# Kernel tuning notes

Measured on AMD Instinct MI355X. Metric: run time of the kernel, lower is better.

## Reference

```python
import jax, jax.numpy as jnp
import numpy as np

# 5-tap binomial kernel, same as torch module
_H5 = jnp.array([0.0625, 0.25, 0.375, 0.25, 0.0625], dtype=jnp.float32)
_K1 = _H5[:, None] * _H5[None, :]        # 5x5 Gaussian, sums to 1 (reduce kernel)
_K4 = 4.0 * _K1                           # expand kernel (gain 4)
# polyphase sub-kernels for expand (match torch strided slicing of kernel)
_KER00 = _K4[0::2, 0::2]  # 3x3
_KER01 = _K4[0::2, 1::2]  # 3x2
_KER10 = _K4[1::2, 0::2]  # 2x3
_KER11 = _K4[1::2, 1::2]  # 2x2


def _dwconv(x, k, stride=1):
    """Depthwise valid conv, same kernel per channel. x: NCHW, k: (kh, kw)."""
    C = x.shape[1]
    kern = jnp.broadcast_to(k[None, None].astype(x.dtype), (C, 1) + k.shape)
    return jax.lax.conv_general_dilated(
        x, kern, (stride, stride), 'VALID',
        dimension_numbers=('NCHW', 'OIHW', 'NCHW'),
        feature_group_count=C)


def pyr_reduce(im):
    # replicate-pad 2 each side, 5x5 conv, subsample [0::2,0::2] == stride-2 conv
    x = jnp.pad(im, ((0, 0), (0, 0), (2, 2), (2, 2)), mode='edge')
    return _dwconv(x, _K1, stride=2)


def pyr_expand(im):
    B, C, H, W = im.shape
    x_r2c2 = jnp.pad(im, ((0, 0), (0, 0), (1, 1), (1, 1)), mode='edge')  # top+bot, left+right
    x_r2c1 = jnp.pad(im, ((0, 0), (0, 0), (1, 1), (0, 1)), mode='edge')  # top+bot, right
    x_c2r1 = jnp.pad(im, ((0, 0), (0, 0), (0, 1), (1, 1)), mode='edge')  # bot, left+right
    x_c1r1 = jnp.pad(im, ((0, 0), (0, 0), (0, 1), (0, 1)), mode='edge')  # bot, right
    o00 = _dwconv(x_r2c2, _KER00)  # -> out[0::2, 0::2]
    o01 = _dwconv(x_r2c1, _KER01)  # -> out[0::2, 1::2]
    o10 = _dwconv(x_c2r1, _KER10)  # -> out[1::2, 0::2]
    o11 = _dwconv(x_c1r1, _KER11)  # -> out[1::2, 1::2]
    out = jnp.zeros((B, C, 2 * H, 2 * W), im.dtype)
    out = out.at[:, :, 0::2, 0::2].set(o00)
    out = out.at[:, :, 0::2, 1::2].set(o01)
    out = out.at[:, :, 1::2, 0::2].set(o10)
    out = out.at[:, :, 1::2, 1::2].set(o11)
    return out


def setup_inputs() -> dict:
    key = jax.random.key(0)
    im = jax.random.normal(key, (16, 3, 1024, 1024), dtype=jnp.float32)
    return {"im": im, "levels": 5}


def reference(im, levels):
    gpyr = [im]
    for _ in range(levels - 1):
        gpyr.append(pyr_reduce(gpyr[-1]))
    lpyr = [gpyr[l] - pyr_expand(gpyr[l + 1]) for l in range(levels - 1)]
    lpyr.append(gpyr[-1])
    return tuple(lpyr)
```

## Files before the change

kernel.cpp:

```cpp
#include <hip/hip_runtime.h>


#define RBX 64
#define RBY 4

typedef float fx4 __attribute__((ext_vector_type(4)));

template <bool EDGE>
__device__ __forceinline__ void reduce_accum(const float* __restrict__ src,
                                             int Hin, int Win, int rbase, int cb,
                                             float (&acc)[4][4]) {
    const float w0 = 0.0625f, w1 = 0.25f, w2 = 0.375f;
    const float wr[5] = {w0, w1, w2, w1, w0};
#pragma unroll
    for (int rr = 0; rr < 11; ++rr) {
        int gr = rbase + rr;
        gr = gr < 0 ? 0 : (gr > Hin - 1 ? Hin - 1 : gr);
        const float* row = src + (size_t)gr * Win;
        float v[16];
        if (!EDGE) {
#pragma unroll
            for (int q = 0; q < 4; ++q) {
                fx4 f = *reinterpret_cast<const fx4*>(row + cb + 4 * q);
                v[4 * q + 0] = f.x; v[4 * q + 1] = f.y;
                v[4 * q + 2] = f.z; v[4 * q + 3] = f.w;
            }
        } else {
#pragma unroll
            for (int c = 0; c < 16; ++c) {
                int gc = cb + c;
                gc = gc < 0 ? 0 : (gc > Win - 1 ? Win - 1 : gc);
                v[c] = row[gc];
            }
        }
        float h[4];
#pragma unroll
        for (int c = 0; c < 4; ++c) {
            const float* vv = v + 2 + 2 * c;
            float s04 = vv[0] + vv[4];
            float s13 = vv[1] + vv[3];
            float hh = w0 * s04;
            hh = fmaf(w1, s13, hh);
            hh = fmaf(w2, vv[2], hh);
            h[c] = hh;
        }
#pragma unroll
        for (int i = 0; i < 4; ++i) {
            const int a = rr - 2 * i;
            if (a >= 0 && a <= 4) {
                const float w = wr[a];
#pragma unroll
                for (int c = 0; c < 4; ++c)
                    acc[i][c] = fmaf(w, h[c], acc[i][c]);
            }
        }
    }
}

__device__ __forceinline__ void reduce_block(const float* __restrict__ src,
                                             float* __restrict__ dst,
                                             int Hin, int Win, int Hout, int Wout,
                                             int bx, int by, int tx, int ty) {
    const int t = bx * RBX + tx;
    const int i0 = (by * RBY + ty) * 4;
    const int j0 = 4 * t;
    if (j0 >= Wout || i0 >= Hout) return;

    const int cb = 8 * t - 4;
    const int rbase = 2 * i0 - 2;
    const bool edge = (cb < 0) | (cb + 15 > Win - 1);

    float acc[4][4];
#pragma unroll
    for (int i = 0; i < 4; ++i)
#pragma unroll
        for (int c = 0; c < 4; ++c) acc[i][c] = 0.f;

    if (!edge) reduce_accum<false>(src, Hin, Win, rbase, cb, acc);
    else       reduce_accum<true>(src, Hin, Win, rbase, cb, acc);

    float* drow = dst + j0;
#pragma unroll
    for (int i = 0; i < 4; ++i) {
        fx4 o = {acc[i][0], acc[i][1], acc[i][2], acc[i][3]};
        *reinterpret_cast<fx4*>(drow + (size_t)(i0 + i) * Wout) = o;
    }
}

__launch_bounds__(256)
__global__ void reduce_kernel(const float* __restrict__ in, float* __restrict__ out,
                              int Hin, int Win, int Hout, int Wout) {
    const int p = blockIdx.z;
    reduce_block(in + (size_t)p * Hin * Win, out + (size_t)p * Hout * Wout,
                 Hin, Win, Hout, Wout, blockIdx.x, blockIdx.y, threadIdx.x, threadIdx.y);
}

template <bool NT>
__device__ __forceinline__ fx4 ld4(const float* p) {
    if (NT) return __builtin_nontemporal_load(reinterpret_cast<const fx4*>(p));
    return *reinterpret_cast<const fx4*>(p);
}
template <bool NT>
__device__ __forceinline__ void st4(float* p, fx4 v) {
    if (NT) __builtin_nontemporal_store(v, reinterpret_cast<fx4*>(p));
    else    *reinterpret_cast<fx4*>(p) = v;
}

template <bool NT>
__device__ __forceinline__ void lap_block(const float* __restrict__ fine,
                                          const float* __restrict__ coarse,
                                          float* __restrict__ out,
                                          int Hc, int Wc, int bx, int by, int tx, int ty) {
    const int t = bx * 64 + tx;
    const int i = by * 4 + ty;
    if (i >= Hc || t >= (Wc >> 2)) return;

    const int im1 = i > 0 ? i - 1 : 0;
    const int ip1 = i < Hc - 1 ? i + 1 : Hc - 1;
    const float* rm = coarse + (size_t)im1 * Wc;
    const float* r0 = coarse + (size_t)i   * Wc;
    const float* rp = coarse + (size_t)ip1 * Wc;

    const int jl = 4 * t - 1 > 0 ? 4 * t - 1 : 0;
    const int jr = 4 * t + 4 < Wc - 1 ? 4 * t + 4 : Wc - 1;

    float cm[6], c0[6], cp[6];
    {
        fx4 m = *reinterpret_cast<const fx4*>(rm + 4 * t);
        fx4 z = *reinterpret_cast<const fx4*>(r0 + 4 * t);
        fx4 q = *reinterpret_cast<const fx4*>(rp + 4 * t);
        cm[1] = m.x; cm[2] = m.y; cm[3] = m.z; cm[4] = m.w;
        c0[1] = z.x; c0[2] = z.y; c0[3] = z.z; c0[4] = z.w;
        cp[1] = q.x; cp[2] = q.y; cp[3] = q.z; cp[4] = q.w;
        cm[0] = rm[jl]; cm[5] = rm[jr];
        c0[0] = r0[jl]; c0[5] = r0[jr];
        cp[0] = rp[jl]; cp[5] = rp[jr];
    }

    float e[6], o[6];
#pragma unroll
    for (int c = 0; c < 6; ++c) {
        e[c] = fmaf(0.125f, cm[c], fmaf(0.75f, c0[c], 0.125f * cp[c]));
        o[c] = 0.5f * (c0[c] + cp[c]);
    }

    float ev[8], ov[8];
#pragma unroll
    for (int q = 0; q < 4; ++q) {
        ev[2 * q]     = fmaf(0.125f, e[q], fmaf(0.75f, e[q + 1], 0.125f * e[q + 2]));
        ev[2 * q + 1] = 0.5f * (e[q + 1] + e[q + 2]);
        ov[2 * q]     = fmaf(0.125f, o[q], fmaf(0.75f, o[q + 1], 0.125f * o[q + 2]));
        ov[2 * q + 1] = 0.5f * (o[q + 1] + o[q + 2]);
    }

    const int Wf = 2 * Wc;
    const size_t r0off = (size_t)(2 * i) * Wf + 8 * t;
    const float* f0 = fine + r0off;
    const float* f1 = f0 + Wf;
    fx4 a0 = ld4<NT>(f0), a1 = ld4<NT>(f0 + 4);
    fx4 b0 = ld4<NT>(f1), b1 = ld4<NT>(f1 + 4);

    float* w0 = out + r0off;
    float* w1 = w0 + Wf;
    fx4 o0 = {a0.x - ev[0], a0.y - ev[1], a0.z - ev[2], a0.w - ev[3]};
    fx4 o1 = {a1.x - ev[4], a1.y - ev[5], a1.z - ev[6], a1.w - ev[7]};
    fx4 o2 = {b0.x - ov[0], b0.y - ov[1], b0.z - ov[2], b0.w - ov[3]};
    fx4 o3 = {b1.x - ov[4], b1.y - ov[5], b1.z - ov[6], b1.w - ov[7]};
    st4<NT>(w0,     o0);
    st4<NT>(w0 + 4, o1);
    st4<NT>(w1,     o2);
    st4<NT>(w1 + 4, o3);
}

__launch_bounds__(256)
__global__ void lap_kernel(const float* __restrict__ fine, const float* __restrict__ coarse,
                           float* __restrict__ out, int Hc, int Wc) {
    const int p = blockIdx.z;
    const size_t mplane = (size_t)Hc * Wc;
    lap_block<false>(fine + (size_t)p * 4 * mplane, coarse + (size_t)p * mplane,
                     out + (size_t)p * 4 * mplane, Hc, Wc,
                     blockIdx.x, blockIdx.y, threadIdx.x, threadIdx.y);
}

template <bool NT>
__launch_bounds__(256)
__global__ void fused_kernel(const float* __restrict__ fine, const float* __restrict__ mid,
                             float* __restrict__ lap_dst, float* __restrict__ red_dst,
                             int Hc, int Wc, int ylap) {
    const int p = blockIdx.z;
    const size_t mplane = (size_t)Hc * Wc;
    if ((int)blockIdx.y < ylap) {
        lap_block<NT>(fine + (size_t)p * 4 * mplane, mid + (size_t)p * mplane,
                      lap_dst + (size_t)p * 4 * mplane, Hc, Wc,
                      blockIdx.x, blockIdx.y, threadIdx.x, threadIdx.y);
    } else {
        reduce_block(mid + (size_t)p * mplane, red_dst + (size_t)p * (mplane >> 2),
                     Hc, Wc, Hc >> 1, Wc >> 1,
                     blockIdx.x, (int)blockIdx.y - ylap, threadIdx.x, threadIdx.y);
    }
}

extern "C" void kernel_launch(void* const* d_in, const int* in_sizes, int n_in,
                              void* d_out, int out_size, void* d_ws, size_t ws_size,
                              hipStream_t stream) {
    (void)in_sizes; (void)n_in; (void)d_ws; (void)ws_size; (void)out_size;
    const float* im = (const float*)d_in[0];
    float* out = (float*)d_out;

    const int P = 48;
    const int H0 = 1024, W0 = 1024;

    size_t off[5];
    size_t acc = 0;
    for (int l = 0; l < 5; ++l) {
        off[l] = acc;
        int h = H0 >> l, w = W0 >> l;
        acc += (size_t)P * h * w;
    }

    {
        int Hout = H0 >> 1, Wout = W0 >> 1;
        dim3 blk(RBX, RBY, 1);
        dim3 grid((Wout + 255) / 256, (Hout + 15) / 16, P);
        reduce_kernel<<<grid, blk, 0, stream>>>(im, out + off[1], H0, W0, Hout, Wout);
    }

    for (int l = 0; l < 3; ++l) {
        int Hc = H0 >> (l + 1), Wc = W0 >> (l + 1);
        int xlap = (Wc / 4 + 63) / 64, ylap = (Hc + 3) / 4;
        int Hout = Hc >> 1, Wout = Wc >> 1;
        int xred = (Wout + 255) / 256, yred = (Hout + 15) / 16;
        dim3 blk(64, 4, 1);
        dim3 grid(xlap > xred ? xlap : xred, ylap + yred, P);
        const float* fine = (l == 0) ? im : (out + off[l]);
        if (l == 0)
            fused_kernel<true><<<grid, blk, 0, stream>>>(fine, out + off[l + 1],
                                                         out + off[l], out + off[l + 2],
                                                         Hc, Wc, ylap);
        else
            fused_kernel<false><<<grid, blk, 0, stream>>>(fine, out + off[l + 1],
                                                          out + off[l], out + off[l + 2],
                                                          Hc, Wc, ylap);
    }

    {
        int Hc = H0 >> 4, Wc = W0 >> 4;
        dim3 blk(64, 4, 1);
        dim3 grid((Wc / 4 + 63) / 64, (Hc + 3) / 4, P);
        lap_kernel<<<grid, blk, 0, stream>>>(out + off[3], out + off[4], out + off[3], Hc, Wc);
    }
}
```

Baseline: 487.6 us.

## Replace multi-kernel pyramid launches with one persistent kernel using grid barriers

Adds a persistent pyr_kernel with 1024 blocks that walk each pyramid stage in grid-stride loops and separate the stages with an atomic-counter global barrier held in the workspace. This removes the four separate kernel launches and their inter-kernel gaps and tail effects. The cost is barrier spin overhead and reliance on all 1024 blocks being co-resident (launch bounds of 4 blocks per CU). The barrier has a spin timeout, so if residency is not met, correctness could break silently. It also adds a memset per call.

```diff
diff --git a/kernel.cpp b/kernel.cpp
--- a/kernel.cpp
+++ b/kernel.cpp
@@ -1,8 +1,5 @@
 #include <hip/hip_runtime.h>
 
-
-#define RBX 64
-#define RBY 4
 
 typedef float fx4 __attribute__((ext_vector_type(4)));
 
@@ -61,8 +58,8 @@
                                              float* __restrict__ dst,
                                              int Hin, int Win, int Hout, int Wout,
                                              int bx, int by, int tx, int ty) {
-    const int t = bx * RBX + tx;
-    const int i0 = (by * RBY + ty) * 4;
+    const int t = bx * 64 + tx;
+    const int i0 = (by * 4 + ty) * 4;
     const int j0 = 4 * t;
     if (j0 >= Wout || i0 >= Hout) return;
 
@@ -85,14 +82,6 @@
         fx4 o = {acc[i][0], acc[i][1], acc[i][2], acc[i][3]};
         *reinterpret_cast<fx4*>(drow + (size_t)(i0 + i) * Wout) = o;
     }
-}
-
-__launch_bounds__(256)
-__global__ void reduce_kernel(const float* __restrict__ in, float* __restrict__ out,
-                              int Hin, int Win, int Hout, int Wout) {
-    const int p = blockIdx.z;
-    reduce_block(in + (size_t)p * Hin * Win, out + (size_t)p * Hout * Wout,
-                 Hin, Win, Hout, Wout, blockIdx.x, blockIdx.y, threadIdx.x, threadIdx.y);
 }
 
 template <bool NT>
@@ -170,6 +159,105 @@
     st4<NT>(w0 + 4, o1);
     st4<NT>(w1,     o2);
     st4<NT>(w1 + 4, o3);
+}
+
+__device__ __forceinline__ void gbar(unsigned* ctr, unsigned target) {
+    __syncthreads();
+    if (threadIdx.x == 0 && threadIdx.y == 0) {
+        __threadfence();
+        __hip_atomic_fetch_add(ctr, 1u, __ATOMIC_ACQ_REL, __HIP_MEMORY_SCOPE_AGENT);
+        unsigned spins = 0;
+        while (__hip_atomic_load(ctr, __ATOMIC_ACQUIRE, __HIP_MEMORY_SCOPE_AGENT) < target) {
+            __builtin_amdgcn_s_sleep(8);
+            if (++spins > 2000000u) break;
+        }
+        __threadfence();
+    }
+    __syncthreads();
+}
+
+#define OFF1 50331648UL
+#define OFF2 62914560UL
+#define OFF3 66060288UL
+#define OFF4 66846720UL
+
+__launch_bounds__(256, 4)
+__global__ void pyr_kernel(const float* __restrict__ im, float* __restrict__ out,
+                           unsigned* ctr) {
+    const int tx = threadIdx.x, ty = threadIdx.y;
+    const unsigned gsz = gridDim.x;
+    const unsigned nblk = gsz;
+
+    for (unsigned bt = blockIdx.x; bt < 3072; bt += gsz) {
+        unsigned p = bt >> 6, r = bt & 63;
+        reduce_block(im + (size_t)p * (1024 * 1024), out + OFF1 + (size_t)p * (512 * 512),
+                     1024, 1024, 512, 512, r & 1, r >> 1, tx, ty);
+    }
+    gbar(ctr, nblk * 1);
+
+    for (unsigned bt = blockIdx.x; bt < 13056; bt += gsz) {
+        if (bt < 12288) {
+            unsigned p = bt >> 8, r = bt & 255;
+            lap_block<true>(im + (size_t)p * (1024 * 1024),
+                            out + OFF1 + (size_t)p * (512 * 512),
+                            out + (size_t)p * (1024 * 1024),
+                            512, 512, r & 1, r >> 1, tx, ty);
+        } else {
+            unsigned b2 = bt - 12288;
+            unsigned p = b2 >> 4, r = b2 & 15;
+            reduce_block(out + OFF1 + (size_t)p * (512 * 512), out + OFF2 + (size_t)p * (256 * 256),
+                         512, 512, 256, 256, 0, r, tx, ty);
+        }
+    }
+    gbar(ctr, nblk * 2);
+
+    for (unsigned bt = blockIdx.x; bt < 3456; bt += gsz) {
+        if (bt < 3072) {
+            unsigned p = bt >> 6, by = bt & 63;
+            lap_block<false>(out + OFF1 + (size_t)p * (512 * 512),
+                             out + OFF2 + (size_t)p * (256 * 256),
+                             out + OFF1 + (size_t)p * (512 * 512),
+                             256, 256, 0, by, tx, ty);
+        } else {
+            unsigned b2 = bt - 3072;
+            unsigned p = b2 >> 3, r = b2 & 7;
+            reduce_block(out + OFF2 + (size_t)p * (256 * 256), out + OFF3 + (size_t)p * (128 * 128),
+                         256, 256, 128, 128, 0, r, tx, ty);
+        }
+    }
+    gbar(ctr, nblk * 3);
+
+    for (unsigned bt = blockIdx.x; bt < 1728; bt += gsz) {
+        if (bt < 1536) {
+            unsigned p = bt >> 5, by = bt & 31;
+            lap_block<false>(out + OFF2 + (size_t)p * (256 * 256),
+                             out + OFF3 + (size_t)p * (128 * 128),
+                             out + OFF2 + (size_t)p * (256 * 256),
+                             128, 128, 0, by, tx, ty);
+        } else {
+            unsigned b2 = bt - 1536;
+            unsigned p = b2 >> 2, r = b2 & 3;
+            reduce_block(out + OFF3 + (size_t)p * (128 * 128), out + OFF4 + (size_t)p * (64 * 64),
+                         128, 128, 64, 64, 0, r, tx, ty);
+        }
+    }
+    gbar(ctr, nblk * 4);
+
+    for (unsigned bt = blockIdx.x; bt < 768; bt += gsz) {
+        unsigned p = bt >> 4, by = bt & 15;
+        lap_block<false>(out + OFF3 + (size_t)p * (128 * 128),
+                         out + OFF4 + (size_t)p * (64 * 64),
+                         out + OFF3 + (size_t)p * (128 * 128),
+                         64, 64, 0, by, tx, ty);
+    }
+}
+
+__launch_bounds__(256)
+__global__ void reduce_kernel(const float* __restrict__ in, float* __restrict__ out,
+                              int Hin, int Win, int Hout, int Wout) {
+    const int p = blockIdx.z;
+    reduce_block(in + (size_t)p * Hin * Win, out + (size_t)p * Hout * Wout,
+                 Hin, Win, Hout, Wout, blockIdx.x, blockIdx.y, threadIdx.x, threadIdx.y);
 }
 
 __launch_bounds__(256)
@@ -203,13 +291,19 @@
 extern "C" void kernel_launch(void* const* d_in, const int* in_sizes, int n_in,
                               void* d_out, int out_size, void* d_ws, size_t ws_size,
                               hipStream_t stream) {
-    (void)in_sizes; (void)n_in; (void)d_ws; (void)ws_size; (void)out_size;
+    (void)in_sizes; (void)n_in; (void)out_size;
     const float* im = (const float*)d_in[0];
     float* out = (float*)d_out;
 
+    if (d_ws != nullptr && ws_size >= 64) {
+        hipMemsetAsync(d_ws, 0, 64, stream);
+        unsigned* ctr = (unsigned*)d_ws;
+        pyr_kernel<<<dim3(1024, 1, 1), dim3(64, 4, 1), 0, stream>>>(im, out, ctr);
+        return;
+    }
+
     const int P = 48;
     const int H0 = 1024, W0 = 1024;
-
     size_t off[5];
     size_t acc = 0;
     for (int l = 0; l < 5; ++l) {
@@ -217,14 +311,12 @@
         int h = H0 >> l, w = W0 >> l;
         acc += (size_t)P * h * w;
     }
-
     {
         int Hout = H0 >> 1, Wout = W0 >> 1;
-        dim3 blk(RBX, RBY, 1);
+        dim3 blk(64, 4, 1);
         dim3 grid((Wout + 255) / 256, (Hout + 15) / 16, P);
         reduce_kernel<<<grid, blk, 0, stream>>>(im, out + off[1], H0, W0, Hout, Wout);
     }
-
     for (int l = 0; l < 3; ++l) {
         int Hc = H0 >> (l + 1), Wc = W0 >> (l + 1);
         int xlap = (Wc / 4 + 63) / 64, ylap = (Hc + 3) / 4;
@@ -242,7 +334,6 @@
                                                           out + off[l], out + off[l + 2],
                                                           Hc, Wc, ylap);
     }
-
     {
         int Hc = H0 >> 4, Wc = W0 >> 4;
         dim3 blk(64, 4, 1);
```

Result: slower. 1.575 ms (+223.0%).
